# Optimization experiments

Hardware: AMD Instinct MI355X
Metric: run time of the kernel (lower is better)

## Reference

```python
import jax, jax.numpy as jnp
import numpy as np

B, C, H, W = 32, 1536, 24, 24
HID, D, K = 512, 128, 64  # hidden, cluster_dim, num_clusters


def setup_inputs() -> dict:
    key = jax.random.key(0)
    ks = jax.random.split(key, 6)
    def rn(k, shape, scale):
        return jax.random.normal(k, shape, dtype=jnp.float32) * scale
    return {
        "x": rn(ks[0], (B, C, H, W), 1.0),
        # cluster_features: Conv2d(C,512,1) -> ReLU -> Conv2d(512,D,1)
        "w1c": rn(ks[1], (HID, C), 0.02), "b1c": jnp.zeros((HID,), jnp.float32),
        "w2c": rn(ks[2], (D, HID), 0.02), "b2c": jnp.zeros((D,), jnp.float32),
        # score: Conv2d(C,512,1) -> ReLU -> Conv2d(512,K,1)
        "w1s": rn(ks[3], (HID, C), 0.02), "b1s": jnp.zeros((HID,), jnp.float32),
        "w2s": rn(ks[4], (K, HID), 0.02), "b2s": jnp.zeros((K,), jnp.float32),
        "temperature": jnp.array(1.0, jnp.float32),
    }


def _sinkhorn_log(S, num_iters=3):
    # log-domain OT solver with uniform marginals log(1/n), reg=1 (M/reg == M)
    b, m, n = S.shape
    norm = -jnp.log(jnp.asarray(n, S.dtype))
    log_a = jnp.full((b, m), norm, S.dtype)
    log_b = jnp.full((b, n), norm, S.dtype)
    u = jnp.zeros((b, m), S.dtype)
    v = jnp.zeros((b, n), S.dtype)
    for _ in range(num_iters):
        u = log_a - jax.nn.logsumexp(S + v[:, None, :], axis=2)
        v = log_b - jax.nn.logsumexp(S + u[:, :, None], axis=1)
    # get_matching_probs subtracts norm at the end
    return S + u[:, :, None] + v[:, None, :] - norm


def reference(x, w1c, b1c, w2c, b2c, w1s, b1s, w2s, b2s, temperature):
    b, c, h, w = x.shape
    xf = x.reshape(b, c, h * w)  # (B, C, N); 1x1 conv == channel GEMM
    # cluster features f: (B, D, N)
    hc = jax.nn.relu(jnp.einsum('oc,bcn->bon', w1c, xf) + b1c[None, :, None])
    f = jnp.einsum('oc,bcn->bon', w2c, hc) + b2c[None, :, None]
    # assignment scores p: (B, K, N)
    hs = jax.nn.relu(jnp.einsum('oc,bcn->bon', w1s, xf) + b1s[None, :, None])
    s = jnp.einsum('oc,bcn->bon', w2s, hs) + b2s[None, :, None]
    log_p = _sinkhorn_log(s, num_iters=3)
    p = jnp.exp(log_p / temperature) + jnp.exp(log_p)  # (B, K, N)
    # (f.unsqueeze(2) * p.unsqueeze(1)).sum(-1) == batched matmul
    agg = jnp.einsum('bcn,bkn->bck', f, p)  # (B, D, K)
    flat = agg.reshape(b, -1)
    nrm = jnp.maximum(jnp.linalg.norm(flat, axis=-1, keepdims=True), 1e-12)
    return flat / nrm
```

## Files before the change

kernel.cpp:

```cpp
#include <hip/hip_runtime.h>

typedef unsigned short ushort_t;
typedef float f32x4 __attribute__((ext_vector_type(4)));
typedef short short8 __attribute__((ext_vector_type(8)));

#define B_   32
#define C_   1536
#define N_   576
#define HID_ 512
#define D_   128
#define K_   64

__device__ __forceinline__ float bf2f(ushort_t u) {
    union { unsigned u; float f; } c; c.u = ((unsigned)u) << 16; return c.f;
}
__device__ __forceinline__ ushort_t f2bf(float x) {
    unsigned u = __float_as_uint(x);
    return (ushort_t)((u + 0x7FFFu + ((u >> 16) & 1u)) >> 16);
}

typedef const __attribute__((address_space(1))) char gas_char;
typedef __attribute__((address_space(3))) char las_char;
__device__ __forceinline__ void cp16(const void* g, void* l) {
    __builtin_amdgcn_global_load_lds((gas_char*)(size_t)g,
                                     (las_char*)(unsigned)(size_t)l, 16, 0, 0);
}

#define OB1_  1572864
#define OW2C_ 1573888
#define OB2C_ 1639424
#define OW2S_ 1639552
#define OB2S_ 1672320
#define WTOT_ 1672384
#define TRB_  6912
#define CVB_  ((WTOT_ + 255) / 256)

__global__ __launch_bounds__(256) void prep_kernel(
    const void* __restrict__ x,
    const void* __restrict__ w1c, const void* __restrict__ b1c,
    const void* __restrict__ w2c, const void* __restrict__ b2c,
    const void* __restrict__ w1s, const void* __restrict__ b1s,
    const void* __restrict__ w2s, const void* __restrict__ b2s,
    const unsigned* __restrict__ temp,
    ushort_t* __restrict__ xt, ushort_t* __restrict__ o, float* __restrict__ Tp)
{
    __shared__ ushort_t t[64][68];
    unsigned d = temp[0];
    int flag = (d == 0x3F800000u) ? 1 : 0;
    int tid = threadIdx.x;
    int idx = blockIdx.x;
    if (idx == 0 && tid == 0)
        *Tp = flag ? __uint_as_float(d) : bf2f((ushort_t)(d & 0xFFFFu));

    if (idx < TRB_) {
        int b = idx / 216, rem = idx % 216;
        int c0 = (rem % 24) * 64, n0 = (rem / 24) * 64;
        ushort_t* xtb = xt + (size_t)b * N_ * C_;
        int r = tid >> 4, c4 = (tid & 15) * 4;
        if (flag) {
            const float* xb = (const float*)x + (size_t)b * C_ * N_;
#pragma unroll
            for (int i = 0; i < 4; ++i) {
                int cc = r + i * 16;
                float4 v = *(const float4*)&xb[(size_t)(c0 + cc) * N_ + n0 + c4];
                t[cc][c4 + 0] = f2bf(v.x);
                t[cc][c4 + 1] = f2bf(v.y);
                t[cc][c4 + 2] = f2bf(v.z);
                t[cc][c4 + 3] = f2bf(v.w);
            }
        } else {
            const ushort_t* xb = (const ushort_t*)x + (size_t)b * C_ * N_;
#pragma unroll
            for (int i = 0; i < 4; ++i) {
                int cc = r + i * 16;
                *(uint2*)&t[cc][c4] =
                    *(const uint2*)&xb[(size_t)(c0 + cc) * N_ + n0 + c4];
            }
        }
        __syncthreads();
#pragma unroll
        for (int i = 0; i < 4; ++i) {
            int nn = r + i * 16;
            ushort_t v0 = t[c4 + 0][nn], v1 = t[c4 + 1][nn];
            ushort_t v2 = t[c4 + 2][nn], v3 = t[c4 + 3][nn];
            uint2 vv;
            vv.x = (unsigned)v0 | ((unsigned)v1 << 16);
            vv.y = (unsigned)v2 | ((unsigned)v3 << 16);
            *(uint2*)&xtb[(size_t)(n0 + nn) * C_ + c0 + c4] = vv;
        }
    } else {
        int i = (idx - TRB_) * 256 + tid;
        if (i >= WTOT_) return;
        const void* p; int off;
        if      (i < 786432)  { p = w1c; off = i; }
        else if (i < OB1_)    { p = w1s; off = i - 786432; }
        else if (i < 1573376) { p = b1c; off = i - OB1_; }
        else if (i < OW2C_)   { p = b1s; off = i - 1573376; }
        else if (i < OB2C_)   { p = w2c; off = i - OW2C_; }
        else if (i < OW2S_)   { p = b2c; off = i - OB2C_; }
        else if (i < OB2S_)   { p = w2s; off = i - OW2S_; }
        else                  { p = b2s; off = i - OB2S_; }
        o[i] = flag ? f2bf(((const float*)p)[off]) : ((const ushort_t*)p)[off];
    }
}

__global__ __launch_bounds__(256) void gemm1_kernel(
    const ushort_t* __restrict__ Xt, const ushort_t* __restrict__ W1,
    const ushort_t* __restrict__ bias, ushort_t* __restrict__ h)
{
    __shared__ ushort_t Atile[128 * 64];
    __shared__ ushort_t Btile[128 * 64];
    int idx = blockIdx.x;
    int l = (idx & 7) * 144 + (idx >> 3);
    int mt = l >> 3, t = l & 7;
    int row0 = mt * 128, col0 = t * 128;

    int tid = threadIdx.x, w = tid >> 6, lane = tid & 63;
    int wr = w >> 1, wc = w & 1;
    int r16 = lane & 15, q = lane >> 4, kh = q * 8;

    int srow = tid >> 3;
    int cx = ((tid & 7) ^ (srow & 7)) * 8;
    const ushort_t* ag[4];
    const ushort_t* bg[4];
#pragma unroll
    for (int s = 0; s < 4; ++s) {
        ag[s] = Xt + (size_t)(row0 + s * 32 + srow) * C_ + cx;
        bg[s] = W1 + (size_t)(col0 + s * 32 + srow) * C_ + cx;
    }
    ushort_t* lA = &Atile[tid * 8];
    ushort_t* lB = &Btile[tid * 8];

    f32x4 acc[4][4];
#pragma unroll
    for (int i = 0; i < 4; ++i)
#pragma unroll
        for (int j = 0; j < 4; ++j) acc[i][j] = f32x4{0.f, 0.f, 0.f, 0.f};

    int rowa = wr * 64 + r16;
    int rowb = wc * 64 + r16;
    int xr = (r16 & 7) * 8;

    for (int k0 = 0; k0 < C_; k0 += 64) {
#pragma unroll
        for (int s = 0; s < 4; ++s) {
            cp16(ag[s], lA + s * 2048);
            cp16(bg[s], lB + s * 2048);
            ag[s] += 64; bg[s] += 64;
        }
        __syncthreads();
#pragma unroll
        for (int ks = 0; ks < 2; ++ks) {
            int ke = (ks * 32 + kh) ^ xr;
            short8 af[4], bf[4];
#pragma unroll
            for (int i = 0; i < 4; ++i)
                af[i] = *(const short8*)&Atile[(rowa + i * 16) * 64 + ke];
#pragma unroll
            for (int j = 0; j < 4; ++j)
                bf[j] = *(const short8*)&Btile[(rowb + j * 16) * 64 + ke];
#pragma unroll
            for (int i = 0; i < 4; ++i)
#pragma unroll
                for (int j = 0; j < 4; ++j)
                    acc[i][j] = __builtin_amdgcn_mfma_f32_16x16x32_bf16(
                        af[i], bf[j], acc[i][j], 0, 0, 0);
        }
        __syncthreads();
    }
#pragma unroll
    for (int j = 0; j < 4; ++j) {
        int col = col0 + wc * 64 + j * 16 + r16;
        float cb = bf2f(bias[col]);
#pragma unroll
        for (int i = 0; i < 4; ++i) {
            int rowo = row0 + wr * 64 + i * 16 + q * 4;
#pragma unroll
            for (int r = 0; r < 4; ++r) {
                float v = fmaxf(acc[i][j][r] + cb, 0.f);
                h[(size_t)(rowo + r) * 1024 + col] = f2bf(v);
            }
        }
    }
}

__global__ __launch_bounds__(256) void gemm2_kernel(
    const ushort_t* __restrict__ Wb, const ushort_t* __restrict__ h,
    ushort_t* __restrict__ fbuf, float* __restrict__ sbuf)
{
    __shared__ ushort_t Atile[128 * 32];
    __shared__ ushort_t Btile[128 * 32];
    int nt = blockIdx.x, b = blockIdx.y, z = blockIdx.z;
    int col0 = nt * 128;
    int Mclamp = z ? K_ : D_;
    const ushort_t* Aw   = Wb + (z ? OW2S_ : OW2C_);
    const ushort_t* bias = Wb + (z ? OB2S_ : OB2C_);
    const ushort_t* hb = h + (size_t)b * N_ * 1024 + (z ? 512 : 0);

    int tid = threadIdx.x, w = tid >> 6, lane = tid & 63;
    int wr = w >> 1, wc = w & 1;
    int r16 = lane & 15, q = lane >> 4, kh = q * 8;

    int ar0 = min((tid >> 2), Mclamp - 1);
    int ar1 = min(64 + (tid >> 2), Mclamp - 1);
    const ushort_t* ag0 = Aw + (size_t)ar0 * HID_ + (tid & 3) * 8;
    const ushort_t* ag1 = Aw + (size_t)ar1 * HID_ + (tid & 3) * 8;
    int br0 = min(col0 + (tid >> 2), N_ - 1);
    int br1 = min(col0 + 64 + (tid >> 2), N_ - 1);
    const ushort_t* bg0 = hb + (size_t)br0 * 1024 + (tid & 3) * 8;
    const ushort_t* bg1 = hb + (size_t)br1 * 1024 + (tid & 3) * 8;
    ushort_t* lA0 = &Atile[w * 512];
    ushort_t* lA1 = &Atile[2048 + w * 512];
    ushort_t* lB0 = &Btile[w * 512];
    ushort_t* lB1 = &Btile[2048 + w * 512];

    f32x4 acc[4][4];
#pragma unroll
    for (int i = 0; i < 4; ++i)
#pragma unroll
        for (int j = 0; j < 4; ++j) acc[i][j] = f32x4{0.f, 0.f, 0.f, 0.f};

    for (int k0 = 0; k0 < HID_; k0 += 32) {
        cp16(ag0, lA0); cp16(ag1, lA1);
        cp16(bg0, lB0); cp16(bg1, lB1);
        ag0 += 32; ag1 += 32; bg0 += 32; bg1 += 32;
        __syncthreads();
        short8 af[4], bf[4];
#pragma unroll
        for (int i = 0; i < 4; ++i)
            af[i] = *(const short8*)&Atile[(wr * 64 + i * 16 + r16) * 32 + kh];
#pragma unroll
        for (int j = 0; j < 4; ++j)
            bf[j] = *(const short8*)&Btile[(wc * 64 + j * 16 + r16) * 32 + kh];
#pragma unroll
        for (int i = 0; i < 4; ++i)
#pragma unroll
            for (int j = 0; j < 4; ++j)
                acc[i][j] = __builtin_amdgcn_mfma_f32_16x16x32_bf16(
                    af[i], bf[j], acc[i][j], 0, 0, 0);
        __syncthreads();
    }
#pragma unroll
    for (int j = 0; j < 4; ++j) {
        int col = col0 + wc * 64 + j * 16 + r16;
#pragma unroll
        for (int i = 0; i < 4; ++i) {
            int rowb = wr * 64 + i * 16 + q * 4;
#pragma unroll
            for (int r = 0; r < 4; ++r) {
                int rr = rowb + r;
                if (rr < Mclamp && col < N_) {
                    float v = acc[i][j][r] + bf2f(bias[rr]);
                    if (z == 0)
                        fbuf[(size_t)b * D_ * N_ + (size_t)rr * N_ + col] = f2bf(v);
                    else
                        sbuf[(size_t)b * K_ * N_ + (size_t)rr * N_ + col] = v;
                }
            }
        }
    }
}

__global__ __launch_bounds__(512) void tail_kernel(
    const ushort_t* __restrict__ f_all, const float* __restrict__ s_all,
    const float* __restrict__ Tp, const unsigned* __restrict__ temp,
    void* __restrict__ out)
{
    int b = blockIdx.x;
    const float* S = s_all + (size_t)b * K_ * N_;
    __shared__ float su[K_];
    __shared__ float sv[N_];
    __shared__ ushort_t Ftile[128 * 32];
    __shared__ ushort_t Ptile[64 * 32];
    __shared__ float red[8];
    int tid = threadIdx.x, w = tid >> 6, lane = tid & 63;
    int r16 = lane & 15, q = lane >> 4, kh = q * 8;
    const float norm = -logf((float)N_);

    for (int n = tid; n < N_; n += 512) sv[n] = 0.f;
    __syncthreads();

    for (int it = 0; it < 3; ++it) {
        for (int r = w; r < K_; r += 8) {
            const float* Sr = S + r * N_;
            float a0 = 0.f, a1 = 0.f, a2 = 0.f;
#pragma unroll
            for (int k = 0; k < 9; k += 3) {
                int n0 = lane + 64 * k;
                a0 += __expf(Sr[n0] + sv[n0]);
                a1 += __expf(Sr[n0 + 64] + sv[n0 + 64]);
                a2 += __expf(Sr[n0 + 128] + sv[n0 + 128]);
            }
            float t = a0 + a1 + a2;
#pragma unroll
            for (int off = 32; off; off >>= 1) t += __shfl_xor(t, off);
            if (lane == 0) su[r] = norm - __logf(t);
        }
        __syncthreads();
        for (int n = tid; n < N_; n += 512) {
            const float* Sc = S + n;
            float a0 = 0.f, a1 = 0.f, a2 = 0.f, a3 = 0.f;
#pragma unroll
            for (int m = 0; m < K_; m += 4) {
                a0 += __expf(Sc[(m + 0) * N_] + su[m + 0]);
                a1 += __expf(Sc[(m + 1) * N_] + su[m + 1]);
                a2 += __expf(Sc[(m + 2) * N_] + su[m + 2]);
                a3 += __expf(Sc[(m + 3) * N_] + su[m + 3]);
            }
            sv[n] = norm - __logf((a0 + a1) + (a2 + a3));
        }
        __syncthreads();
    }

    float invT = 1.f / (*Tp);
    const ushort_t* f = f_all + (size_t)b * D_ * N_;
    const ushort_t* fg = f + (size_t)(tid >> 2) * N_ + (tid & 3) * 8;
    ushort_t* lF = &Ftile[tid * 8];
    int prow = tid >> 3, pc0 = (tid & 7) * 4;
    float urow = su[prow];
    const float* Srow = S + (size_t)prow * N_ + pc0;

    f32x4 acc[4];
#pragma unroll
    for (int j = 0; j < 4; ++j) acc[j] = f32x4{0.f, 0.f, 0.f, 0.f};

    for (int s = 0; s < 18; ++s) {
        cp16(fg, lF);
        fg += 32;
        int nb = s * 32;
        ushort_t pv[4];
#pragma unroll
        for (int e = 0; e < 4; ++e) {
            float lp = Srow[e] + urow + sv[nb + pc0 + e] - norm;
            pv[e] = f2bf(__expf(lp * invT) + __expf(lp));
        }
        Srow += 32;
        uint2 w0;
        w0.x = (unsigned)pv[0] | ((unsigned)pv[1] << 16);
        w0.y = (unsigned)pv[2] | ((unsigned)pv[3] << 16);
        *(uint2*)&Ptile[prow * 32 + pc0] = w0;
        __syncthreads();
        short8 af = *(const short8*)&Ftile[(w * 16 + r16) * 32 + kh];
        short8 bf[4];
#pragma unroll
        for (int j = 0; j < 4; ++j)
            bf[j] = *(const short8*)&Ptile[(j * 16 + r16) * 32 + kh];
#pragma unroll
        for (int j = 0; j < 4; ++j)
            acc[j] = __builtin_amdgcn_mfma_f32_16x16x32_bf16(
                af, bf[j], acc[j], 0, 0, 0);
        __syncthreads();
    }

    float ssq = 0.f;
#pragma unroll
    for (int j = 0; j < 4; ++j)
#pragma unroll
        for (int r = 0; r < 4; ++r) { float v = acc[j][r]; ssq += v * v; }
#pragma unroll
    for (int off = 32; off; off >>= 1) ssq += __shfl_xor(ssq, off);
    if (lane == 0) red[w] = ssq;
    __syncthreads();
    float tot = (red[0] + red[1] + red[2] + red[3])
              + (red[4] + red[5] + red[6] + red[7]);
    float inv = 1.f / fmaxf(sqrtf(tot), 1e-12f);
    int flag = (temp[0] == 0x3F800000u) ? 1 : 0;
#pragma unroll
    for (int j = 0; j < 4; ++j) {
        int col = j * 16 + r16;
#pragma unroll
        for (int r = 0; r < 4; ++r) {
            int row = w * 16 + q * 4 + r;
            float v = acc[j][r] * inv;
            size_t idx = (size_t)b * D_ * K_ + (size_t)row * K_ + col;
            if (flag) ((float*)out)[idx] = v;
            else      ((ushort_t*)out)[idx] = f2bf(v);
        }
    }
}

extern "C" void kernel_launch(void* const* d_in, const int* in_sizes, int n_in,
                              void* d_out, int out_size, void* d_ws, size_t ws_size,
                              hipStream_t stream) {
    const void* x    = d_in[0];
    const void* w1c  = d_in[1];
    const void* b1c  = d_in[2];
    const void* w2c  = d_in[3];
    const void* b2c  = d_in[4];
    const void* w1s  = d_in[5];
    const void* b1s  = d_in[6];
    const void* w2s  = d_in[7];
    const void* b2s  = d_in[8];
    const unsigned* temp = (const unsigned*)d_in[9];

    char* ws = (char*)d_ws;
    float* Tp = (float*)ws;
    ushort_t* Wb = (ushort_t*)(ws + 256);
    size_t offXt = 256 + (((size_t)WTOT_ * 2 + 255) & ~(size_t)255);
    ushort_t* Xt = (ushort_t*)(ws + offXt);
    size_t xtBytes = (size_t)B_ * N_ * C_ * 2;
    ushort_t* h  = (ushort_t*)(ws + offXt + xtBytes);
    size_t o0 = offXt;
    ushort_t* fbuf = (ushort_t*)(ws + o0);  o0 += (size_t)B_ * D_ * N_ * 2;
    float*    sbuf = (float*)(ws + o0);     o0 += (size_t)B_ * K_ * N_ * 4;

    prep_kernel<<<dim3(TRB_ + CVB_), 256, 0, stream>>>(
        x, w1c, b1c, w2c, b2c, w1s, b1s, w2s, b2s, temp, Xt, Wb, Tp);
    gemm1_kernel<<<dim3(1152), 256, 0, stream>>>(Xt, Wb, Wb + OB1_, h);
    gemm2_kernel<<<dim3(5, B_, 2), 256, 0, stream>>>(Wb, h, fbuf, sbuf);
    tail_kernel<<<dim3(B_), 512, 0, stream>>>(fbuf, sbuf, Tp, temp, (void*)d_out);
}
```

Before: 326.7 us.

## Double-buffer GEMM tiles, vectorize weight conversion, split tail into sinkhorn/agg/norm kernels

Both GEMM kernels now use double-buffered LDS tiles with async global-to-LDS copies, waiting on vmcnt so the next K-slice loads while the current one computes. gemm2 also gains an XOR swizzle on its LDS layout to reduce bank conflicts. The weight conversion in prep is vectorized to four elements per thread. The single-block-per-batch tail kernel is split into a sinkhorn kernel, an aggregation kernel spread over 8 blocks per batch, and a normalization kernel, which raises parallelism at the cost of extra launches and workspace round trips.

```diff
diff --git a/kernel.cpp b/kernel.cpp
--- a/kernel.cpp
+++ b/kernel.cpp
@@ -24,6 +24,11 @@
 __device__ __forceinline__ void cp16(const void* g, void* l) {
     __builtin_amdgcn_global_load_lds((gas_char*)(size_t)g,
                                      (las_char*)(unsigned)(size_t)l, 16, 0, 0);
+}
+__device__ __forceinline__ void bar() {
+    asm volatile("" ::: "memory");
+    __builtin_amdgcn_s_barrier();
+    asm volatile("" ::: "memory");
 }
 
 #define OB1_  1572864
@@ -33,7 +38,7 @@
 #define OB2S_ 1672320
 #define WTOT_ 1672384
 #define TRB_  6912
-#define CVB_  ((WTOT_ + 255) / 256)
+#define CVB4_ (((WTOT_ / 4) + 255) / 256)
 
 __global__ __launch_bounds__(256) void prep_kernel(
     const void* __restrict__ x,
@@ -89,18 +94,26 @@
             *(uint2*)&xtb[(size_t)(n0 + nn) * C_ + c0 + c4] = vv;
         }
     } else {
-        int i = (idx - TRB_) * 256 + tid;
-        if (i >= WTOT_) return;
+        int i4 = ((idx - TRB_) * 256 + tid) * 4;
+        if (i4 >= WTOT_) return;
         const void* p; int off;
-        if      (i < 786432)  { p = w1c; off = i; }
-        else if (i < OB1_)    { p = w1s; off = i - 786432; }
-        else if (i < 1573376) { p = b1c; off = i - OB1_; }
-        else if (i < OW2C_)   { p = b1s; off = i - 1573376; }
-        else if (i < OB2C_)   { p = w2c; off = i - OW2C_; }
-        else if (i < OW2S_)   { p = b2c; off = i - OB2C_; }
-        else if (i < OB2S_)   { p = w2s; off = i - OW2S_; }
-        else                  { p = b2s; off = i - OB2S_; }
-        o[i] = flag ? f2bf(((const float*)p)[off]) : ((const ushort_t*)p)[off];
+        if      (i4 < 786432)  { p = w1c; off = i4; }
+        else if (i4 < OB1_)    { p = w1s; off = i4 - 786432; }
+        else if (i4 < 1573376) { p = b1c; off = i4 - OB1_; }
+        else if (i4 < OW2C_)   { p = b1s; off = i4 - 1573376; }
+        else if (i4 < OB2C_)   { p = w2c; off = i4 - OW2C_; }
+        else if (i4 < OW2S_)   { p = b2c; off = i4 - OB2C_; }
+        else if (i4 < OB2S_)   { p = w2s; off = i4 - OW2S_; }
+        else                   { p = b2s; off = i4 - OB2S_; }
+        if (flag) {
+            float4 v = *(const float4*)((const float*)p + off);
+            uint2 r;
+            r.x = (unsigned)f2bf(v.x) | ((unsigned)f2bf(v.y) << 16);
+            r.y = (unsigned)f2bf(v.z) | ((unsigned)f2bf(v.w) << 16);
+            *(uint2*)&o[i4] = r;
+        } else {
+            *(uint2*)&o[i4] = *(const uint2*)((const ushort_t*)p + off);
+        }
     }
 }
 
@@ -108,8 +121,8 @@
     const ushort_t* __restrict__ Xt, const ushort_t* __restrict__ W1,
     const ushort_t* __restrict__ bias, ushort_t* __restrict__ h)
 {
-    __shared__ ushort_t Atile[128 * 64];
-    __shared__ ushort_t Btile[128 * 64];
+    __shared__ ushort_t Atile[2][128 * 64];
+    __shared__ ushort_t Btile[2][128 * 64];
     int idx = blockIdx.x;
     int l = (idx & 7) * 144 + (idx >> 3);
     int mt = l >> 3, t = l & 7;
@@ -128,8 +141,6 @@
         ag[s] = Xt + (size_t)(row0 + s * 32 + srow) * C_ + cx;
         bg[s] = W1 + (size_t)(col0 + s * 32 + srow) * C_ + cx;
     }
-    ushort_t* lA = &Atile[tid * 8];
-    ushort_t* lB = &Btile[tid * 8];
 
     f32x4 acc[4][4];
 #pragma unroll
@@ -141,24 +152,25 @@
     int rowb = wc * 64 + r16;
     int xr = (r16 & 7) * 8;
 
-    for (int k0 = 0; k0 < C_; k0 += 64) {
+    auto stage = [&](int buf) {
 #pragma unroll
         for (int s = 0; s < 4; ++s) {
-            cp16(ag[s], lA + s * 2048);
-            cp16(bg[s], lB + s * 2048);
+            cp16(ag[s], &Atile[buf][tid * 8 + s * 2048]);
+            cp16(bg[s], &Btile[buf][tid * 8 + s * 2048]);
             ag[s] += 64; bg[s] += 64;
         }
-        __syncthreads();
+    };
+    auto compute = [&](int cb) {
 #pragma unroll
         for (int ks = 0; ks < 2; ++ks) {
             int ke = (ks * 32 + kh) ^ xr;
             short8 af[4], bf[4];
 #pragma unroll
             for (int i = 0; i < 4; ++i)
-                af[i] = *(const short8*)&Atile[(rowa + i * 16) * 64 + ke];
+                af[i] = *(const short8*)&Atile[cb][(rowa + i * 16) * 64 + ke];
 #pragma unroll
             for (int j = 0; j < 4; ++j)
-                bf[j] = *(const short8*)&Btile[(rowb + j * 16) * 64 + ke];
+                bf[j] = *(const short8*)&Btile[cb][(rowb + j * 16) * 64 + ke];
 #pragma unroll
             for (int i = 0; i < 4; ++i)
 #pragma unroll
@@ -166,8 +178,22 @@
                     acc[i][j] = __builtin_amdgcn_mfma_f32_16x16x32_bf16(
                         af[i], bf[j], acc[i][j], 0, 0, 0);
         }
-        __syncthreads();
-    }
+    };
+
+    stage(0);
+    int cur = 0;
+    for (int kt = 0; kt < 23; ++kt) {
+        stage(cur ^ 1);
+        asm volatile("s_waitcnt vmcnt(8)" ::: "memory");
+        bar();
+        compute(cur);
+        bar();
+        cur ^= 1;
+    }
+    asm volatile("s_waitcnt vmcnt(0)" ::: "memory");
+    bar();
+    compute(cur);
+
 #pragma unroll
     for (int j = 0; j < 4; ++j) {
         int col = col0 + wc * 64 + j * 16 + r16;
@@ -188,8 +214,8 @@
     const ushort_t* __restrict__ Wb, const ushort_t* __restrict__ h,
     ushort_t* __restrict__ fbuf, float* __restrict__ sbuf)
 {
-    __shared__ ushort_t Atile[128 * 32];
-    __shared__ ushort_t Btile[128 * 32];
+    __shared__ ushort_t Atile[2][128 * 32];
+    __shared__ ushort_t Btile[2][128 * 32];
     int nt = blockIdx.x, b = blockIdx.y, z = blockIdx.z;
     int col0 = nt * 128;
     int Mclamp = z ? K_ : D_;
@@ -201,18 +227,16 @@
     int wr = w >> 1, wc = w & 1;
     int r16 = lane & 15, q = lane >> 4, kh = q * 8;
 
-    int ar0 = min((tid >> 2), Mclamp - 1);
-    int ar1 = min(64 + (tid >> 2), Mclamp - 1);
-    const ushort_t* ag0 = Aw + (size_t)ar0 * HID_ + (tid & 3) * 8;
-    const ushort_t* ag1 = Aw + (size_t)ar1 * HID_ + (tid & 3) * 8;
-    int br0 = min(col0 + (tid >> 2), N_ - 1);
-    int br1 = min(col0 + 64 + (tid >> 2), N_ - 1);
-    const ushort_t* bg0 = hb + (size_t)br0 * 1024 + (tid & 3) * 8;
-    const ushort_t* bg1 = hb + (size_t)br1 * 1024 + (tid & 3) * 8;
-    ushort_t* lA0 = &Atile[w * 512];
-    ushort_t* lA1 = &Atile[2048 + w * 512];
-    ushort_t* lB0 = &Btile[w * 512];
-    ushort_t* lB1 = &Btile[2048 + w * 512];
+    int srow = tid >> 2;
+    int swz = ((tid & 3) ^ (srow & 3)) * 8;
+    int ar0 = min(srow, Mclamp - 1);
+    int ar1 = min(64 + srow, Mclamp - 1);
+    const ushort_t* ag0 = Aw + (size_t)ar0 * HID_ + swz;
+    const ushort_t* ag1 = Aw + (size_t)ar1 * HID_ + swz;
+    int br0 = min(col0 + srow, N_ - 1);
+    int br1 = min(col0 + 64 + srow, N_ - 1);
+    const ushort_t* bg0 = hb + (size_t)br0 * 1024 + swz;
+    const ushort_t* bg1 = hb + (size_t)br1 * 1024 + swz;
 
     f32x4 acc[4][4];
 #pragma unroll
@@ -220,26 +244,46 @@
 #pragma unroll
         for (int j = 0; j < 4; ++j) acc[i][j] = f32x4{0.f, 0.f, 0.f, 0.f};
 
-    for (int k0 = 0; k0 < HID_; k0 += 32) {
-        cp16(ag0, lA0); cp16(ag1, lA1);
-        cp16(bg0, lB0); cp16(bg1, lB1);
+    int xr = (r16 & 3) * 8;
+
+    auto stage = [&](int buf) {
+        cp16(ag0, &Atile[buf][tid * 8]);
+        cp16(ag1, &Atile[buf][2048 + tid * 8]);
+        cp16(bg0, &Btile[buf][tid * 8]);
+        cp16(bg1, &Btile[buf][2048 + tid * 8]);
         ag0 += 32; ag1 += 32; bg0 += 32; bg1 += 32;
-        __syncthreads();
+    };
+    auto compute = [&](int cb) {
+        int ke = kh ^ xr;
         short8 af[4], bf[4];
 #pragma unroll
         for (int i = 0; i < 4; ++i)
-            af[i] = *(const short8*)&Atile[(wr * 64 + i * 16 + r16) * 32 + kh];
+            af[i] = *(const short8*)&Atile[cb][(wr * 64 + i * 16 + r16) * 32 + ke];
 #pragma unroll
         for (int j = 0; j < 4; ++j)
-            bf[j] = *(const short8*)&Btile[(wc * 64 + j * 16 + r16) * 32 + kh];
+            bf[j] = *(const short8*)&Btile[cb][(wc * 64 + j * 16 + r16) * 32 + ke];
 #pragma unroll
         for (int i = 0; i < 4; ++i)
 #pragma unroll
             for (int j = 0; j < 4; ++j)
                 acc[i][j] = __builtin_amdgcn_mfma_f32_16x16x32_bf16(
                     af[i], bf[j], acc[i][j], 0, 0, 0);
-        __syncthreads();
-    }
+    };
+
+    stage(0);
+    int cur = 0;
+    for (int kt = 0; kt < 15; ++kt) {
+        stage(cur ^ 1);
+        asm volatile("s_waitcnt vmcnt(4)" ::: "memory");
+        bar();
+        compute(cur);
+        bar();
+        cur ^= 1;
+    }
+    asm volatile("s_waitcnt vmcnt(0)" ::: "memory");
+    bar();
+    compute(cur);
+
 #pragma unroll
     for (int j = 0; j < 4; ++j) {
         int col = col0 + wc * 64 + j * 16 + r16;
@@ -261,20 +305,14 @@
     }
 }
 
-__global__ __launch_bounds__(512) void tail_kernel(
-    const ushort_t* __restrict__ f_all, const float* __restrict__ s_all,
-    const float* __restrict__ Tp, const unsigned* __restrict__ temp,
-    void* __restrict__ out)
+__global__ __launch_bounds__(512) void sinkhorn_kernel(
+    const float* __restrict__ s_all, float* __restrict__ uv)
 {
     int b = blockIdx.x;
     const float* S = s_all + (size_t)b * K_ * N_;
     __shared__ float su[K_];
     __shared__ float sv[N_];
-    __shared__ ushort_t Ftile[128 * 32];
-    __shared__ ushort_t Ptile[64 * 32];
-    __shared__ float red[8];
     int tid = threadIdx.x, w = tid >> 6, lane = tid & 63;
-    int r16 = lane & 15, q = lane >> 4, kh = q * 8;
     const float norm = -logf((float)N_);
 
     for (int n = tid; n < N_; n += 512) sv[n] = 0.f;
@@ -311,70 +349,110 @@
         }
         __syncthreads();
     }
+    float* ub = uv + (size_t)b * 640;
+    if (tid < K_) ub[tid] = su[tid];
+    for (int n = tid; n < N_; n += 512) ub[64 + n] = sv[n];
+}
+
+__global__ __launch_bounds__(256) void agg_kernel(
+    const ushort_t* __restrict__ f_all, const float* __restrict__ s_all,
+    const float* __restrict__ uv, const float* __restrict__ Tp,
+    float* __restrict__ aggws)
+{
+    int rblk = blockIdx.x;
+    int b = blockIdx.y;
+    const float* S = s_all + (size_t)b * K_ * N_;
+    __shared__ float su[K_];
+    __shared__ float sv[N_];
+    __shared__ ushort_t Ftile[16 * 32];
+    __shared__ ushort_t Ptile[64 * 32];
+    int tid = threadIdx.x, w = tid >> 6, lane = tid & 63;
+    int r16 = lane & 15, q = lane >> 4;
+    const float norm = -logf((float)N_);
+    const float* ub = uv + (size_t)b * 640;
+    if (tid < K_) su[tid] = ub[tid];
+    for (int n = tid; n < N_; n += 256) sv[n] = ub[64 + n];
+    __syncthreads();
 
     float invT = 1.f / (*Tp);
-    const ushort_t* f = f_all + (size_t)b * D_ * N_;
-    const ushort_t* fg = f + (size_t)(tid >> 2) * N_ + (tid & 3) * 8;
-    ushort_t* lF = &Ftile[tid * 8];
-    int prow = tid >> 3, pc0 = (tid & 7) * 4;
+    const ushort_t* f = f_all + (size_t)b * D_ * N_ + (size_t)(rblk * 16) * N_;
+    int frow = tid >> 2, fch = tid & 3;
+    const ushort_t* fg = f + (size_t)frow * N_ + (size_t)((fch ^ (frow & 3)) * 8);
+    int prow = tid >> 2, pc0 = (tid & 3) * 8;
+    int pswz = ((tid & 3) ^ (prow & 3)) * 8;
     float urow = su[prow];
     const float* Srow = S + (size_t)prow * N_ + pc0;
-
-    f32x4 acc[4];
-#pragma unroll
-    for (int j = 0; j < 4; ++j) acc[j] = f32x4{0.f, 0.f, 0.f, 0.f};
+    int xa = (q ^ (r16 & 3)) * 8;
+
+    f32x4 acc = f32x4{0.f, 0.f, 0.f, 0.f};
 
     for (int s = 0; s < 18; ++s) {
-        cp16(fg, lF);
+        if (tid < 64) cp16(fg, &Ftile[tid * 8]);
         fg += 32;
         int nb = s * 32;
-        ushort_t pv[4];
-#pragma unroll
-        for (int e = 0; e < 4; ++e) {
+        ushort_t pv[8];
+#pragma unroll
+        for (int e = 0; e < 8; ++e) {
             float lp = Srow[e] + urow + sv[nb + pc0 + e] - norm;
             pv[e] = f2bf(__expf(lp * invT) + __expf(lp));
         }
         Srow += 32;
-        uint2 w0;
+        uint2 w0, w1;
         w0.x = (unsigned)pv[0] | ((unsigned)pv[1] << 16);
         w0.y = (unsigned)pv[2] | ((unsigned)pv[3] << 16);
-        *(uint2*)&Ptile[prow * 32 + pc0] = w0;
+        w1.x = (unsigned)pv[4] | ((unsigned)pv[5] << 16);
+        w1.y = (unsigned)pv[6] | ((unsigned)pv[7] << 16);
+        *(uint2*)&Ptile[prow * 32 + pswz] = w0;
+        *(uint2*)&Ptile[prow * 32 + pswz + 4] = w1;
         __syncthreads();
-        short8 af = *(const short8*)&Ftile[(w * 16 + r16) * 32 + kh];
-        short8 bf[4];
-#pragma unroll
-        for (int j = 0; j < 4; ++j)
-            bf[j] = *(const short8*)&Ptile[(j * 16 + r16) * 32 + kh];
-#pragma unroll
-        for (int j = 0; j < 4; ++j)
-            acc[j] = __builtin_amdgcn_mfma_f32_16x16x32_bf16(
-                af, bf[j], acc[j], 0, 0, 0);
+        short8 af = *(const short8*)&Ftile[r16 * 32 + xa];
+        short8 bf = *(const short8*)&Ptile[(w * 16 + r16) * 32 + xa];
+        acc = __builtin_amdgcn_mfma_f32_16x16x32_bf16(af, bf, acc, 0, 0, 0);
         __syncthreads();
     }
-
+    float* ao = aggws + (size_t)b * (D_ * K_) + (size_t)(rblk * 16) * K_ + (w * 16 + r16);
+#pragma unroll
+    for (int r = 0; r < 4; ++r)
+        ao[(size_t)(q * 4 + r) * K_] = acc[r];
+}
+
+__global__ __launch_bounds__(256) void norm_kernel(
+    const float* __restrict__ aggws, const unsigned* __restrict__ temp,
+    void* __restrict__ out)
+{
+    int b = blockIdx.x, tid = threadIdx.x, w = tid >> 6, lane = tid & 63;
+    __shared__ float red[4];
+    const float4* a4 = (const float4*)(aggws + (size_t)b * (D_ * K_));
+    float4 v[8];
     float ssq = 0.f;
 #pragma unroll
-    for (int j = 0; j < 4; ++j)
-#pragma unroll
-        for (int r = 0; r < 4; ++r) { float v = acc[j][r]; ssq += v * v; }
+    for (int i = 0; i < 8; ++i) {
+        v[i] = a4[tid + i * 256];
+        ssq += v[i].x * v[i].x + v[i].y * v[i].y + v[i].z * v[i].z + v[i].w * v[i].w;
+    }
 #pragma unroll
     for (int off = 32; off; off >>= 1) ssq += __shfl_xor(ssq, off);
     if (lane == 0) red[w] = ssq;
     __syncthreads();
-    float tot = (red[0] + red[1] + red[2] + red[3])
-              + (red[4] + red[5] + red[6] + red[7]);
+    float tot = red[0] + red[1] + red[2] + red[3];
     float inv = 1.f / fmaxf(sqrtf(tot), 1e-12f);
     int flag = (temp[0] == 0x3F800000u) ? 1 : 0;
-#pragma unroll
-    for (int j = 0; j < 4; ++j) {
-        int col = j * 16 + r16;
-#pragma unroll
-        for (int r = 0; r < 4; ++r) {
-            int row = w * 16 + q * 4 + r;
-            float v = acc[j][r] * inv;
-            size_t idx = (size_t)b * D_ * K_ + (size_t)row * K_ + col;
-            if (flag) ((float*)out)[idx] = v;
-            else      ((ushort_t*)out)[idx] = f2bf(v);
+    if (flag) {
+        float4* o4 = (float4*)out + (size_t)b * 2048;
+#pragma unroll
+        for (int i = 0; i < 8; ++i) {
+            float4 t = v[i];
+            t.x *= inv; t.y *= inv; t.z *= inv; t.w *= inv;
+            o4[tid + i * 256] = t;
+        }
+    } else {
+        ushort_t* ob = (ushort_t*)out + (size_t)b * 8192;
+#pragma unroll
+        for (int i = 0; i < 8; ++i) {
+            uint2 p;
+            p.x = (unsigned)f2bf(v[i].x * inv) | ((unsigned)f2bf(v[i].y * inv) << 16);
+            p.y = (unsigned)f2bf(v[i].z * inv) | ((unsigned)f2bf(v[i].w * inv) << 16);
+            *(uint2*)&ob[(size_t)(tid + i * 256) * 4] = p;
         }
     }
 }
@@ -399,14 +477,19 @@
     size_t offXt = 256 + (((size_t)WTOT_ * 2 + 255) & ~(size_t)255);
     ushort_t* Xt = (ushort_t*)(ws + offXt);
     size_t xtBytes = (size_t)B_ * N_ * C_ * 2;
+    size_t hBytes  = (size_t)B_ * N_ * 1024 * 2;
     ushort_t* h  = (ushort_t*)(ws + offXt + xtBytes);
     size_t o0 = offXt;
     ushort_t* fbuf = (ushort_t*)(ws + o0);  o0 += (size_t)B_ * D_ * N_ * 2;
     float*    sbuf = (float*)(ws + o0);     o0 += (size_t)B_ * K_ * N_ * 4;
-
-    prep_kernel<<<dim3(TRB_ + CVB_), 256, 0, stream>>>(
+    float* uvws  = (float*)(ws + offXt + xtBytes + hBytes);
+    float* aggws = uvws + (size_t)B_ * 640;
+
+    prep_kernel<<<dim3(TRB_ + CVB4_), 256, 0, stream>>>(
         x, w1c, b1c, w2c, b2c, w1s, b1s, w2s, b2s, temp, Xt, Wb, Tp);
     gemm1_kernel<<<dim3(1152), 256, 0, stream>>>(Xt, Wb, Wb + OB1_, h);
     gemm2_kernel<<<dim3(5, B_, 2), 256, 0, stream>>>(Wb, h, fbuf, sbuf);
-    tail_kernel<<<dim3(B_), 512, 0, stream>>>(fbuf, sbuf, Tp, temp, (void*)d_out);
-}
+    sinkhorn_kernel<<<dim3(B_), 512, 0, stream>>>(sbuf, uvws);
+    agg_kernel<<<dim3(8, B_), 256, 0, stream>>>(fbuf, sbuf, uvws, Tp, aggws);
+    norm_kernel<<<dim3(B_), 256, 0, stream>>>(aggws, temp, (void*)d_out);
+}
```

Result: faster. 314.7 us (-3.6%).
